# Kernel tuning notes

Hardware: AMD Instinct MI355X
Metric: run time of the kernel (lower is better)

## Reference

```python
import jax, jax.numpy as jnp
import numpy as np

BATCH, NUM_FEAT, EMB = 1024, 32, 16
HIDDEN = [128, 128, 128]


def setup_inputs() -> dict:
    key = jax.random.key(0)
    ks = jax.random.split(key, 4)
    inputs = jax.random.normal(ks[0], (BATCH, NUM_FEAT, EMB), dtype=jnp.float32)
    # Conv1D kernel_size=1 -> dense weight of shape (in_dim, units) per layer.
    # in_dim_i = h_{i-1} * num_feat, with h_{-1} = num_feat.
    in0 = NUM_FEAT * NUM_FEAT          # 1024
    in1 = HIDDEN[0] * NUM_FEAT         # 4096
    in2 = HIDDEN[1] * NUM_FEAT         # 4096
    scale = lambda fan_in: (1.0 / np.sqrt(fan_in)).astype(np.float32) if isinstance(fan_in, np.ndarray) else np.float32(1.0 / np.sqrt(fan_in))
    W0 = jax.random.normal(ks[1], (in0, HIDDEN[0]), dtype=jnp.float32) * scale(in0)
    W1 = jax.random.normal(ks[2], (in1, HIDDEN[1]), dtype=jnp.float32) * scale(in1)
    W2 = jax.random.normal(ks[3], (in2, HIDDEN[2]), dtype=jnp.float32) * scale(in2)
    b0 = jnp.zeros((HIDDEN[0],), dtype=jnp.float32)
    b1 = jnp.zeros((HIDDEN[1],), dtype=jnp.float32)
    b2 = jnp.zeros((HIDDEN[2],), dtype=jnp.float32)
    return {"inputs": inputs, "W0": W0, "b0": b0, "W1": W1, "b1": b1, "W2": W2, "b2": b2}


def reference(inputs, W0, b0, W1, b1, W2, b2):
    # inputs: (b, m, e) -> x0: (b, e, m)  [channels-last like tf.transpose perm=[0,2,1]]
    x0 = jnp.transpose(inputs, (0, 2, 1))
    b, d, m = x0.shape
    params = [(W0, b0), (W1, b1), (W2, b2)]
    xl = x0
    layer_outs = []
    for i, (W, bias) in enumerate(params):
        h = xl.shape[-1]
        # outer product over feature axes: (b, d, h, m) -> flatten to (b, d, h*m)
        zl = jnp.einsum('bdh,bdm->bdhm', xl, x0).reshape(b, d, h * m)
        xl = zl @ W + bias  # 1x1 conv == per-position GEMM
        if i < len(params) - 1:
            xl = jax.nn.relu(xl)
        layer_outs.append(xl)
    # sum over embedding axis d, concat over layers -> (b, sum(HIDDEN))
    return jnp.concatenate([o.sum(axis=1) for o in layer_outs], axis=1)
```

## Files before the change

kernel.cpp:

```cpp
#include <hip/hip_runtime.h>


typedef unsigned int u32;
typedef __attribute__((ext_vector_type(8))) short short8;
typedef __attribute__((ext_vector_type(4))) float f32x4;
typedef __attribute__((ext_vector_type(4))) u32 u32x4;

#define R_TOTAL 16384

union PackU { u32 u[4]; short8 s; };
union PackB { u32x4 v; short8 s; };

__device__ __forceinline__ u32 pack_rne(float a, float b) {
  u32 r;
  asm("v_cvt_pk_bf16_f32 %0, %1, %2" : "=v"(r) : "v"(a), "v"(b));
  return r;
}

__device__ __forceinline__ void build_x0t_body(const float* __restrict__ in,
                                               float* __restrict__ x0t,
                                               int bid, int tid, float* t) {
  const int b0 = bid * 8;
  #pragma unroll
  for (int rep = 0; rep < 4; ++rep) {
    int idx = tid + rep * 256;
    *(float4*)&t[idx * 4] = *(const float4*)&in[(size_t)b0 * 512 + idx * 4];
  }
  __syncthreads();
  #pragma unroll
  for (int rep = 0; rep < 4; ++rep) {
    int idx = tid + rep * 256;
    int m = idx >> 5, rem = idx & 31;
    int bl = rem >> 2, dq = rem & 3;
    float4 v = *(const float4*)&t[bl * 512 + m * 16 + dq * 4];
    const int rb = b0 + bl;
    float* dst = &x0t[(size_t)m * R_TOTAL + (rb >> 2) * 64 + (rb & 3)];
    dst[(dq * 4 + 0) * 4] = v.x;
    dst[(dq * 4 + 1) * 4] = v.y;
    dst[(dq * 4 + 2) * 4] = v.z;
    dst[(dq * 4 + 3) * 4] = v.w;
  }
}

__device__ __forceinline__ void swizzle_body(const float* __restrict__ W,
                                             u32* __restrict__ wt,
                                             int bid, int tid, float* wl) {
  const int t = bid >> 2, nq = bid & 3;
  {
    int kk = tid >> 3, c4 = tid & 7;
    float4 v = *(const float4*)&W[(size_t)(t * 32 + kk) * 128 + nq * 32 + c4 * 4];
    wl[kk * 33 + c4 * 4 + 0] = v.x;
    wl[kk * 33 + c4 * 4 + 1] = v.y;
    wl[kk * 33 + c4 * 4 + 2] = v.z;
    wl[kk * 33 + c4 * 4 + 3] = v.w;
  }
  __syncthreads();
  if (tid < 128) {
    int nl = tid >> 2, p = tid & 3;
    int q = p ^ (nl & 3);
    u32 o[4];
    #pragma unroll
    for (int jj = 0; jj < 4; ++jj)
      o[jj] = pack_rne(wl[(q * 8 + 2 * jj + 0) * 33 + nl],
                       wl[(q * 8 + 2 * jj + 1) * 33 + nl]);
    *(u32x4*)(wt + (size_t)(t * 4 + nq) * 512 + nl * 16 + p * 4) =
        u32x4{o[0], o[1], o[2], o[3]};
  }
}

__global__ __launch_bounds__(256) void prep_all(
    const float* __restrict__ in, float* __restrict__ x0t,
    const float* __restrict__ W0, u32* __restrict__ wt0,
    const float* __restrict__ W1, u32* __restrict__ wt1,
    const float* __restrict__ W2, u32* __restrict__ wt2) {
  __shared__ float sh[4096];
  const int b = blockIdx.x, tid = threadIdx.x;
  if (b < 128)      build_x0t_body(in, x0t, b, tid, sh);
  else if (b < 256) swizzle_body(W0, wt0, b - 128, tid, sh);
  else if (b < 768) swizzle_body(W1, wt1, b - 256, tid, sh);
  else              swizzle_body(W2, wt2, b - 768, tid, sh);
}

#define KITER(I, SLOT, DO_ISSUE, BP)                                           \
  {                                                                            \
    PackU Z[4];                                                                \
    _Pragma("unroll")                                                          \
    for (int f = 0; f < 4; ++f) {                                              \
      const float xs = xlv[SLOT][f];                                           \
      _Pragma("unroll")                                                        \
      for (int jj = 0; jj < 4; ++jj)                                           \
        Z[f].u[jj] = pack_rne(xs * x0v[f][2 * jj], xs * x0v[f][2 * jj + 1]);   \
    }                                                                          \
    _Pragma("unroll")                                                          \
    for (int f = 0; f < 4; ++f)                                                \
      acc[f][0] = __builtin_amdgcn_mfma_f32_16x16x32_bf16(Z[f].s, BP[0].s, acc[f][0], 0, 0, 0); \
    _Pragma("unroll")                                                          \
    for (int f = 0; f < 4; ++f)                                                \
      acc[f][1] = __builtin_amdgcn_mfma_f32_16x16x32_bf16(Z[f].s, BP[1].s, acc[f][1], 0, 0, 0); \
    if (DO_ISSUE) {                                                            \
      const u32* ib = wt + (size_t)((t0 + (I) + 2) * 4 + nq) * 512;            \
      BP[0].v = *(const u32x4*)(ib + boff0);                                   \
      BP[1].v = *(const u32x4*)(ib + boff1);                                   \
      xlv[SLOT] = *(const f32x4*)(xt + (size_t)(t0 + (I) + 2) * R_TOTAL +      \
                                  r0 + ln15 * 4);                              \
    }                                                                          \
  }

template <int NT, bool RELU, bool STORE_X>
__global__ __launch_bounds__(512, 2) void layer_mfma(
    const float* __restrict__ xt,
    const float* __restrict__ x0t,
    const u32* __restrict__ wt,
    const float* __restrict__ bias,
    float* __restrict__ xoutT,
    float* __restrict__ osum)
{
  constexpr int HT = NT / 2;
  static_assert((HT & 1) == 0 && HT >= 4, "pair-loop needs even HT >= 4");
  __shared__ u32 smem[16384];

  const int tid = threadIdx.x;
  const int w = tid >> 6, lane = tid & 63;
  const int ln15 = lane & 15, q = lane >> 4;
  const int kh = w & 1, nq = w >> 1;
  const int r0 = blockIdx.x * 64;
  const int sw = ln15 & 3;
  u32* mybuf = smem + w * 2048;

  const int boff0 = ln15 * 16 + ((q ^ sw) * 4);
  const int boff1 = (16 + ln15) * 16 + ((q ^ sw) * 4);

  float x0v[4][8];
  #pragma unroll
  for (int f = 0; f < 4; ++f) {
    #pragma unroll
    for (int j = 0; j < 8; ++j)
      x0v[f][j] = x0t[(size_t)(q * 8 + j) * R_TOTAL + r0 + ln15 * 4 + f];
  }

  f32x4 acc[4][2];
  #pragma unroll
  for (int f = 0; f < 4; ++f)
    #pragma unroll
    for (int c = 0; c < 2; ++c) acc[f][c] = f32x4{0.f, 0.f, 0.f, 0.f};

  const int t0 = kh * HT;

  PackB ba[2], bb[2];
  f32x4 xlv[2];
  {
    const u32* ib = wt + (size_t)(t0 * 4 + nq) * 512;
    ba[0].v = *(const u32x4*)(ib + boff0);
    ba[1].v = *(const u32x4*)(ib + boff1);
    xlv[0] = *(const f32x4*)(xt + (size_t)t0 * R_TOTAL + r0 + ln15 * 4);
  }
  {
    const u32* ib = wt + (size_t)((t0 + 1) * 4 + nq) * 512;
    bb[0].v = *(const u32x4*)(ib + boff0);
    bb[1].v = *(const u32x4*)(ib + boff1);
    xlv[1] = *(const f32x4*)(xt + (size_t)(t0 + 1) * R_TOTAL + r0 + ln15 * 4);
  }

  for (int i = 0; i < HT - 2; i += 2) {
    KITER(i,     0, 1, ba);
    KITER(i + 1, 1, 1, bb);
  }
  KITER(HT - 2, 0, 0, ba);
  KITER(HT - 1, 1, 0, bb);

  __syncthreads();
  if (kh == 1) {
    u32* reg = mybuf;
    #pragma unroll
    for (int f = 0; f < 4; ++f)
      #pragma unroll
      for (int c = 0; c < 2; ++c)
        *(f32x4*)(reg + ((size_t)(f * 2 + c) * 64 + lane) * 4) = acc[f][c];
  }
  __syncthreads();
  if (kh == 0) {
    const u32* reg = smem + (w + 1) * 2048;
    float bs[2];
    #pragma unroll
    for (int c = 0; c < 2; ++c) bs[c] = bias[nq * 32 + c * 16 + ln15];

    f32x4 vv[4][2];
    #pragma unroll
    for (int f = 0; f < 4; ++f) {
      #pragma unroll
      for (int c = 0; c < 2; ++c) {
        f32x4 part = *(const f32x4*)(reg + ((size_t)(f * 2 + c) * 64 + lane) * 4);
        f32x4 v = acc[f][c] + part;
        v.x += bs[c]; v.y += bs[c]; v.z += bs[c]; v.w += bs[c];
        if (RELU) {
          v.x = fmaxf(v.x, 0.f); v.y = fmaxf(v.y, 0.f);
          v.z = fmaxf(v.z, 0.f); v.w = fmaxf(v.w, 0.f);
        }
        vv[f][c] = v;
        float s = v.x + v.y + v.z + v.w;
        s += __shfl_xor(s, 16, 64);
        s += __shfl_xor(s, 32, 64);
        if (q == 0)
          osum[(size_t)((r0 >> 4) + f) * 384 + nq * 32 + c * 16 + ln15] = s;
      }
    }

    if (STORE_X) {
      u32* myreg = mybuf;
      #pragma unroll
      for (int f = 0; f < 4; ++f)
        #pragma unroll
        for (int c = 0; c < 2; ++c)
          *(f32x4*)(myreg + ((size_t)(f * 2 + c) * 64 + lane) * 4) = vv[f][c];
      const int i15 = lane & 15;
      #pragma unroll
      for (int c = 0; c < 2; ++c) {
        #pragma unroll
        for (int rr = 0; rr < 4; ++rr) {
          const int colIdx = (lane >> 4) + rr * 4;
          float o[4];
          #pragma unroll
          for (int f = 0; f < 4; ++f)
            o[f] = *(const float*)(myreg + (size_t)(f * 2 + c) * 256 +
                                   ((i15 >> 2) * 16 + colIdx) * 4 + (i15 & 3));
          const int col = nq * 32 + c * 16 + colIdx;
          *(f32x4*)&xoutT[(size_t)col * R_TOTAL + r0 + i15 * 4] =
              f32x4{o[0], o[1], o[2], o[3]};
        }
      }
    }
  }
}

extern "C" void kernel_launch(void* const* d_in, const int* in_sizes, int n_in,
                              void* d_out, int out_size, void* d_ws, size_t ws_size,
                              hipStream_t stream) {
  const float* in = (const float*)d_in[0];
  const float* W0 = (const float*)d_in[1];
  const float* b0 = (const float*)d_in[2];
  const float* W1 = (const float*)d_in[3];
  const float* b1 = (const float*)d_in[4];
  const float* W2 = (const float*)d_in[5];
  const float* b2 = (const float*)d_in[6];
  float* out = (float*)d_out;

  float* X0T = (float*)d_ws;
  float* X1T = X0T + (size_t)32 * R_TOTAL;
  float* X2T = X1T + (size_t)128 * R_TOTAL;
  u32* Wt0 = (u32*)(X2T + (size_t)128 * R_TOTAL);
  u32* Wt1 = Wt0 + (size_t)32 * 4 * 512;
  u32* Wt2 = Wt1 + (size_t)128 * 4 * 512;

  prep_all<<<1280, 256, 0, stream>>>(in, X0T, W0, Wt0, W1, Wt1, W2, Wt2);

  layer_mfma<32, true, true><<<256, 512, 0, stream>>>(X0T, X0T, Wt0, b0, X1T, out + 0);
  layer_mfma<128, true, true><<<256, 512, 0, stream>>>(X1T, X0T, Wt1, b1, X2T, out + 128);
  layer_mfma<128, false, false><<<256, 512, 0, stream>>>(X2T, X0T, Wt2, b2, nullptr, out + 256);
}
```

Measured before the change: 128.5 us.

## Fuse three CIN layer kernels into one with activations kept in LDS

Replaces the three per-layer MFMA launches with a single kernel that runs all three layers back to back per 64-row block. Intermediate activations (128 columns x 64 rows) are stored in shared memory instead of being written to and read back from global workspace. This removes two kernel launches and the global round trip of the X1/X2 activations. The cost is extra block-wide barriers and LDS traffic, with 64KB of shared memory per block that may limit occupancy.

Measured after the change: 118.3 us. 7.9% less time.

```diff
diff --git a/kernel.cpp b/kernel.cpp
--- a/kernel.cpp
+++ b/kernel.cpp
@@ -81,42 +81,124 @@
   else              swizzle_body(W2, wt2, b - 768, tid, sh);
 }
 
-#define KITER(I, SLOT, DO_ISSUE, BP)                                           \
-  {                                                                            \
-    PackU Z[4];                                                                \
-    _Pragma("unroll")                                                          \
-    for (int f = 0; f < 4; ++f) {                                              \
-      const float xs = xlv[SLOT][f];                                           \
-      _Pragma("unroll")                                                        \
-      for (int jj = 0; jj < 4; ++jj)                                           \
-        Z[f].u[jj] = pack_rne(xs * x0v[f][2 * jj], xs * x0v[f][2 * jj + 1]);   \
-    }                                                                          \
-    _Pragma("unroll")                                                          \
-    for (int f = 0; f < 4; ++f)                                                \
-      acc[f][0] = __builtin_amdgcn_mfma_f32_16x16x32_bf16(Z[f].s, BP[0].s, acc[f][0], 0, 0, 0); \
-    _Pragma("unroll")                                                          \
-    for (int f = 0; f < 4; ++f)                                                \
-      acc[f][1] = __builtin_amdgcn_mfma_f32_16x16x32_bf16(Z[f].s, BP[1].s, acc[f][1], 0, 0, 0); \
-    if (DO_ISSUE) {                                                            \
-      const u32* ib = wt + (size_t)((t0 + (I) + 2) * 4 + nq) * 512;            \
-      BP[0].v = *(const u32x4*)(ib + boff0);                                   \
-      BP[1].v = *(const u32x4*)(ib + boff1);                                   \
-      xlv[SLOT] = *(const f32x4*)(xt + (size_t)(t0 + (I) + 2) * R_TOTAL +      \
-                                  r0 + ln15 * 4);                              \
-    }                                                                          \
-  }
-
-template <int NT, bool RELU, bool STORE_X>
-__global__ __launch_bounds__(512, 2) void layer_mfma(
-    const float* __restrict__ xt,
-    const float* __restrict__ x0t,
-    const u32* __restrict__ wt,
-    const float* __restrict__ bias,
-    float* __restrict__ xoutT,
-    float* __restrict__ osum)
+template <int NT, bool RELU, bool STORE_X, bool XL_LDS>
+__device__ __forceinline__ void run_phase(
+    const float* __restrict__ xg, const float* al,
+    const u32* __restrict__ wt, const float* __restrict__ bias,
+    float* __restrict__ osum, u32* smem, float* actW,
+    const float (&x0v)[4][8],
+    int w, int lane, int ln15, int q, int kh, int nq, int r0,
+    int boff0, int boff1)
 {
   constexpr int HT = NT / 2;
   static_assert((HT & 1) == 0 && HT >= 4, "pair-loop needs even HT >= 4");
+
+  f32x4 acc[4][2];
+  #pragma unroll
+  for (int f = 0; f < 4; ++f)
+    #pragma unroll
+    for (int c = 0; c < 2; ++c) acc[f][c] = f32x4{0.f, 0.f, 0.f, 0.f};
+
+  const int t0 = kh * HT;
+
+  PackB ba[2], bb[2];
+  f32x4 xlv[2];
+  {
+    const u32* ib = wt + (size_t)(t0 * 4 + nq) * 512;
+    ba[0].v = *(const u32x4*)(ib + boff0);
+    ba[1].v = *(const u32x4*)(ib + boff1);
+    if constexpr (XL_LDS) xlv[0] = *(const f32x4*)(al + t0 * 64 + ln15 * 4);
+    else xlv[0] = *(const f32x4*)(xg + (size_t)t0 * R_TOTAL + r0 + ln15 * 4);
+  }
+  {
+    const u32* ib = wt + (size_t)((t0 + 1) * 4 + nq) * 512;
+    bb[0].v = *(const u32x4*)(ib + boff0);
+    bb[1].v = *(const u32x4*)(ib + boff1);
+    if constexpr (XL_LDS) xlv[1] = *(const f32x4*)(al + (t0 + 1) * 64 + ln15 * 4);
+    else xlv[1] = *(const f32x4*)(xg + (size_t)(t0 + 1) * R_TOTAL + r0 + ln15 * 4);
+  }
+
+  auto kit = [&](int I, int SLOT, bool issue, PackB (&BP)[2]) {
+    PackU Z[4];
+    #pragma unroll
+    for (int f = 0; f < 4; ++f) {
+      const float xs = xlv[SLOT][f];
+      #pragma unroll
+      for (int jj = 0; jj < 4; ++jj)
+        Z[f].u[jj] = pack_rne(xs * x0v[f][2 * jj], xs * x0v[f][2 * jj + 1]);
+    }
+    #pragma unroll
+    for (int f = 0; f < 4; ++f)
+      acc[f][0] = __builtin_amdgcn_mfma_f32_16x16x32_bf16(Z[f].s, BP[0].s, acc[f][0], 0, 0, 0);
+    #pragma unroll
+    for (int f = 0; f < 4; ++f)
+      acc[f][1] = __builtin_amdgcn_mfma_f32_16x16x32_bf16(Z[f].s, BP[1].s, acc[f][1], 0, 0, 0);
+    if (issue) {
+      const int t = t0 + I + 2;
+      const u32* ib = wt + (size_t)(t * 4 + nq) * 512;
+      BP[0].v = *(const u32x4*)(ib + boff0);
+      BP[1].v = *(const u32x4*)(ib + boff1);
+      if constexpr (XL_LDS) xlv[SLOT] = *(const f32x4*)(al + t * 64 + ln15 * 4);
+      else xlv[SLOT] = *(const f32x4*)(xg + (size_t)t * R_TOTAL + r0 + ln15 * 4);
+    }
+  };
+
+  for (int i = 0; i < HT - 2; i += 2) {
+    kit(i, 0, true, ba);
+    kit(i + 1, 1, true, bb);
+  }
+  kit(HT - 2, 0, false, ba);
+  kit(HT - 1, 1, false, bb);
+
+  __syncthreads();
+  u32* dmp = smem + (size_t)(w >> 1) * 2048;
+  if (kh == 1) {
+    #pragma unroll
+    for (int f = 0; f < 4; ++f)
+      #pragma unroll
+      for (int c = 0; c < 2; ++c)
+        *(f32x4*)(dmp + ((size_t)(f * 2 + c) * 64 + lane) * 4) = acc[f][c];
+  }
+  __syncthreads();
+  if (kh == 0) {
+    float bs[2];
+    #pragma unroll
+    for (int c = 0; c < 2; ++c) bs[c] = bias[nq * 32 + c * 16 + ln15];
+    #pragma unroll
+    for (int f = 0; f < 4; ++f) {
+      #pragma unroll
+      for (int c = 0; c < 2; ++c) {
+        f32x4 part = *(const f32x4*)(dmp + ((size_t)(f * 2 + c) * 64 + lane) * 4);
+        f32x4 v = acc[f][c] + part;
+        v.x += bs[c]; v.y += bs[c]; v.z += bs[c]; v.w += bs[c];
+        if (RELU) {
+          v.x = fmaxf(v.x, 0.f); v.y = fmaxf(v.y, 0.f);
+          v.z = fmaxf(v.z, 0.f); v.w = fmaxf(v.w, 0.f);
+        }
+        float s = v.x + v.y + v.z + v.w;
+        s += __shfl_xor(s, 16, 64);
+        s += __shfl_xor(s, 32, 64);
+        if (q == 0)
+          osum[(size_t)((r0 >> 4) + f) * 384 + nq * 32 + c * 16 + ln15] = s;
+        if (STORE_X) {
+          const int colb = (nq * 32 + c * 16 + ln15) * 64 + f;
+          #pragma unroll
+          for (int rr = 0; rr < 4; ++rr)
+            actW[colb + (q * 4 + rr) * 4] = v[rr];
+        }
+      }
+    }
+  }
+}
+
+__global__ __launch_bounds__(512, 2) void fused_cin(
+    const float* __restrict__ x0t,
+    const u32* __restrict__ wt0, const u32* __restrict__ wt1,
+    const u32* __restrict__ wt2,
+    const float* __restrict__ b0, const float* __restrict__ b1,
+    const float* __restrict__ b2,
+    float* __restrict__ out)
+{
   __shared__ u32 smem[16384];
 
   const int tid = threadIdx.x;
@@ -125,111 +207,30 @@
   const int kh = w & 1, nq = w >> 1;
   const int r0 = blockIdx.x * 64;
   const int sw = ln15 & 3;
-  u32* mybuf = smem + w * 2048;
 
   const int boff0 = ln15 * 16 + ((q ^ sw) * 4);
   const int boff1 = (16 + ln15) * 16 + ((q ^ sw) * 4);
 
+  float* actF = (float*)(smem + 8192);
+
   float x0v[4][8];
   #pragma unroll
-  for (int f = 0; f < 4; ++f) {
+  for (int f = 0; f < 4; ++f)
     #pragma unroll
     for (int j = 0; j < 8; ++j)
       x0v[f][j] = x0t[(size_t)(q * 8 + j) * R_TOTAL + r0 + ln15 * 4 + f];
-  }
-
-  f32x4 acc[4][2];
-  #pragma unroll
-  for (int f = 0; f < 4; ++f)
-    #pragma unroll
-    for (int c = 0; c < 2; ++c) acc[f][c] = f32x4{0.f, 0.f, 0.f, 0.f};
-
-  const int t0 = kh * HT;
-
-  PackB ba[2], bb[2];
-  f32x4 xlv[2];
-  {
-    const u32* ib = wt + (size_t)(t0 * 4 + nq) * 512;
-    ba[0].v = *(const u32x4*)(ib + boff0);
-    ba[1].v = *(const u32x4*)(ib + boff1);
-    xlv[0] = *(const f32x4*)(xt + (size_t)t0 * R_TOTAL + r0 + ln15 * 4);
-  }
-  {
-    const u32* ib = wt + (size_t)((t0 + 1) * 4 + nq) * 512;
-    bb[0].v = *(const u32x4*)(ib + boff0);
-    bb[1].v = *(const u32x4*)(ib + boff1);
-    xlv[1] = *(const f32x4*)(xt + (size_t)(t0 + 1) * R_TOTAL + r0 + ln15 * 4);
-  }
-
-  for (int i = 0; i < HT - 2; i += 2) {
-    KITER(i,     0, 1, ba);
-    KITER(i + 1, 1, 1, bb);
-  }
-  KITER(HT - 2, 0, 0, ba);
-  KITER(HT - 1, 1, 0, bb);
-
-  __syncthreads();
-  if (kh == 1) {
-    u32* reg = mybuf;
-    #pragma unroll
-    for (int f = 0; f < 4; ++f)
-      #pragma unroll
-      for (int c = 0; c < 2; ++c)
-        *(f32x4*)(reg + ((size_t)(f * 2 + c) * 64 + lane) * 4) = acc[f][c];
-  }
-  __syncthreads();
-  if (kh == 0) {
-    const u32* reg = smem + (w + 1) * 2048;
-    float bs[2];
-    #pragma unroll
-    for (int c = 0; c < 2; ++c) bs[c] = bias[nq * 32 + c * 16 + ln15];
-
-    f32x4 vv[4][2];
-    #pragma unroll
-    for (int f = 0; f < 4; ++f) {
-      #pragma unroll
-      for (int c = 0; c < 2; ++c) {
-        f32x4 part = *(const f32x4*)(reg + ((size_t)(f * 2 + c) * 64 + lane) * 4);
-        f32x4 v = acc[f][c] + part;
-        v.x += bs[c]; v.y += bs[c]; v.z += bs[c]; v.w += bs[c];
-        if (RELU) {
-          v.x = fmaxf(v.x, 0.f); v.y = fmaxf(v.y, 0.f);
-          v.z = fmaxf(v.z, 0.f); v.w = fmaxf(v.w, 0.f);
-        }
-        vv[f][c] = v;
-        float s = v.x + v.y + v.z + v.w;
-        s += __shfl_xor(s, 16, 64);
-        s += __shfl_xor(s, 32, 64);
-        if (q == 0)
-          osum[(size_t)((r0 >> 4) + f) * 384 + nq * 32 + c * 16 + ln15] = s;
-      }
-    }
-
-    if (STORE_X) {
-      u32* myreg = mybuf;
-      #pragma unroll
-      for (int f = 0; f < 4; ++f)
-        #pragma unroll
-        for (int c = 0; c < 2; ++c)
-          *(f32x4*)(myreg + ((size_t)(f * 2 + c) * 64 + lane) * 4) = vv[f][c];
-      const int i15 = lane & 15;
-      #pragma unroll
-      for (int c = 0; c < 2; ++c) {
-        #pragma unroll
-        for (int rr = 0; rr < 4; ++rr) {
-          const int colIdx = (lane >> 4) + rr * 4;
-          float o[4];
-          #pragma unroll
-          for (int f = 0; f < 4; ++f)
-            o[f] = *(const float*)(myreg + (size_t)(f * 2 + c) * 256 +
-                                   ((i15 >> 2) * 16 + colIdx) * 4 + (i15 & 3));
-          const int col = nq * 32 + c * 16 + colIdx;
-          *(f32x4*)&xoutT[(size_t)col * R_TOTAL + r0 + i15 * 4] =
-              f32x4{o[0], o[1], o[2], o[3]};
-        }
-      }
-    }
-  }
+
+  run_phase<32, true, true, false>(x0t, nullptr, wt0, b0, out + 0,
+                                   smem, actF, x0v,
+                                   w, lane, ln15, q, kh, nq, r0, boff0, boff1);
+  __syncthreads();
+  run_phase<128, true, true, true>(nullptr, actF, wt1, b1, out + 128,
+                                   smem, actF, x0v,
+                                   w, lane, ln15, q, kh, nq, r0, boff0, boff1);
+  __syncthreads();
+  run_phase<128, false, false, true>(nullptr, actF, wt2, b2, out + 256,
+                                     smem, actF, x0v,
+                                     w, lane, ln15, q, kh, nq, r0, boff0, boff1);
 }
 
 extern "C" void kernel_launch(void* const* d_in, const int* in_sizes, int n_in,
@@ -245,15 +246,11 @@
   float* out = (float*)d_out;
 
   float* X0T = (float*)d_ws;
-  float* X1T = X0T + (size_t)32 * R_TOTAL;
-  float* X2T = X1T + (size_t)128 * R_TOTAL;
-  u32* Wt0 = (u32*)(X2T + (size_t)128 * R_TOTAL);
+  u32* Wt0 = (u32*)(X0T + (size_t)32 * R_TOTAL);
   u32* Wt1 = Wt0 + (size_t)32 * 4 * 512;
   u32* Wt2 = Wt1 + (size_t)128 * 4 * 512;
 
   prep_all<<<1280, 256, 0, stream>>>(in, X0T, W0, Wt0, W1, Wt1, W2, Wt2);
 
-  layer_mfma<32, true, true><<<256, 512, 0, stream>>>(X0T, X0T, Wt0, b0, X1T, out + 0);
-  layer_mfma<128, true, true><<<256, 512, 0, stream>>>(X1T, X0T, Wt1, b1, X2T, out + 128);
-  layer_mfma<128, false, false><<<256, 512, 0, stream>>>(X2T, X0T, Wt2, b2, nullptr, out + 256);
-}
+  fused_cin<<<256, 512, 0, stream>>>(X0T, Wt0, Wt1, Wt2, b0, b1, b2, out);
+}
```
